# Kernel tuning notes

Measured on AMD Instinct MI355X. Metric: run time of the kernel, lower is better.

## Reference

```python
import jax, jax.numpy as jnp
import numpy as np

B, N, C, DK, TOPK = 4, 4096, 256, 64, 8


def setup_inputs() -> dict:
    key = jax.random.key(0)
    k1, k2, k3 = jax.random.split(key, 3)
    x = jax.random.normal(k1, (B, N, C), dtype=jnp.float32)
    # nn.Linear(channels, d_k, bias=False) weights, stored as [C, DK] for x @ W
    W_q = jax.random.normal(k2, (C, DK), dtype=jnp.float32) * (C ** -0.5)
    W_k = jax.random.normal(k3, (C, DK), dtype=jnp.float32) * (C ** -0.5)
    return {"x": x, "W_q": W_q, "W_k": W_k, "top_k": TOPK}


def reference(x, W_q, W_k, top_k):
    d_k = W_q.shape[-1]
    scale = d_k ** -0.5
    Q = x @ W_q                                   # [B, N, DK]
    K = x @ W_k                                   # [B, N, DK]
    S = jnp.einsum('bnd,bmd->bnm', Q, K) * scale  # [B, N, N]
    _, topk_idx = jax.lax.top_k(S, top_k)         # [B, N, top_k]
    n = S.shape[-1]
    # scatter True at top-k column indices per row (mirrors torch scatter_)
    row_mask = lambda idx: jnp.zeros((n,), dtype=bool).at[idx].set(True)
    mask = jax.vmap(jax.vmap(row_mask))(topk_idx)  # [B, N, N] bool
    S_masked = jnp.where(mask, S, -jnp.inf)
    A = jax.nn.softmax(S_masked, axis=-1)
    return A
```

## Files before the change

### kernel.cpp

```cpp
#include <hip/hip_runtime.h>
#include <math.h>

#define NROW 16384
#define NCOL 4096
#define CDIM 256
#define DKDIM 64
#define SCALE 0.125f

typedef float v4f __attribute__((ext_vector_type(4)));
typedef __attribute__((ext_vector_type(8))) short short8v;
typedef __attribute__((ext_vector_type(4))) float f32x4;

__device__ __forceinline__ unsigned mono(float v) {
  unsigned u = __float_as_uint(v);
  unsigned s = (unsigned)(((int)u) >> 31);
  return u ^ (s | 0x80000000u);
}
__device__ __forceinline__ float unmono(unsigned k) {
  unsigned u = (k & 0x80000000u) ? (k ^ 0x80000000u) : ~k;
  return __uint_as_float(u);
}
__device__ __forceinline__ unsigned short f2bf(float f) {
  unsigned u = __float_as_uint(f);
  u += 0x7FFFu + ((u >> 16) & 1u);
  return (unsigned short)(u >> 16);
}
__device__ __forceinline__ unsigned umaxu(unsigned a, unsigned b) { return a > b ? a : b; }

__device__ __forceinline__ void ins8(unsigned tk[8], unsigned& tmin, int& tmpos, unsigned v) {
  #pragma unroll
  for (int j = 0; j < 8; ++j) if (j == tmpos) tk[j] = v;
  tmin = tk[0]; tmpos = 0;
  #pragma unroll
  for (int j = 1; j < 8; ++j) if (tk[j] < tmin) { tmin = tk[j]; tmpos = j; }
}
__device__ __forceinline__ unsigned umax8(const unsigned kv[8]) {
  unsigned a = umaxu(umaxu(kv[0], kv[1]), umaxu(kv[2], kv[3]));
  unsigned b = umaxu(umaxu(kv[4], kv[5]), umaxu(kv[6], kv[7]));
  return umaxu(a, b);
}
__device__ __forceinline__ void seed8r(const unsigned kv[8],
                                       unsigned tk[8], unsigned& tmin, int& tmpos) {
  #pragma unroll
  for (int j = 0; j < 8; ++j) tk[j] = kv[j];
  tmin = tk[0]; tmpos = 0;
  #pragma unroll
  for (int j = 1; j < 8; ++j) if (tk[j] < tmin) { tmin = tk[j]; tmpos = j; }
}
__device__ __forceinline__ void scan8r(const unsigned kvin[8],
                                       unsigned tk[8], unsigned& tmin, int& tmpos) {
  unsigned kv[8];
  #pragma unroll
  for (int j = 0; j < 8; ++j) kv[j] = kvin[j];
  unsigned gm = umax8(kv);
  #pragma unroll
  for (int pass = 0; pass < 2; ++pass) {
    if (__any(gm > tmin)) {
      if (gm > tmin) {
        ins8(tk, tmin, tmpos, gm);
        #pragma unroll
        for (int j = 0; j < 8; ++j) if (kv[j] == gm) kv[j] = 0u;
      }
      gm = umax8(kv);
    }
  }
  if (__any(gm > tmin)) {
    #pragma unroll
    for (int j = 0; j < 8; ++j) if (kv[j] > tmin) ins8(tk, tmin, tmpos, kv[j]);
  }
}

__device__ __forceinline__ int kswz(int row, int off) {
  return row * 512 + (off ^ (((off >> 6) & 7) << 2));
}
__device__ __forceinline__ void ld8swz(const unsigned* k, int row, int off,
                                       unsigned kv[8]) {
  uint4 ka = *(const uint4*)&k[kswz(row, off)];
  uint4 kb = *(const uint4*)&k[kswz(row, off + 4)];
  kv[0] = ka.x; kv[1] = ka.y; kv[2] = ka.z; kv[3] = ka.w;
  kv[4] = kb.x; kv[5] = kb.y; kv[6] = kb.z; kv[7] = kb.w;
}

__global__ __launch_bounds__(512, 2) void qk_proj(
    const float* __restrict__ x, const float* __restrict__ Wq,
    const float* __restrict__ Wk, float* __restrict__ Qt,
    float* __restrict__ Kt, unsigned short* __restrict__ Qh,
    unsigned short* __restrict__ Kh) {
  __shared__ float4 xs4[64][65];
  const int t = threadIdx.x;
  const int rb = blockIdx.x;
  {
    const float4* xg = (const float4*)(x + (size_t)rb * 64 * CDIM);
    #pragma unroll
    for (int i = 0; i < 8; ++i) {
      int idx = i * 512 + t;
      xs4[idx >> 6][idx & 63] = xg[idx];
    }
  }
  __syncthreads();

  const int lane = t & 63;
  const int wu = __builtin_amdgcn_readfirstlane(t >> 6);
  const int proj = wu >> 2;
  const int chunk = wu & 3;
  const float* __restrict__ Wp = proj ? Wk : Wq;

  float acc[16];
  #pragma unroll
  for (int j = 0; j < 16; ++j) acc[j] = 0.f;

  #pragma unroll 4
  for (int cs = 0; cs < 64; ++cs) {
    float4 xv = xs4[lane][cs];
    const float xc[4] = {xv.x, xv.y, xv.z, xv.w};
    #pragma unroll
    for (int i = 0; i < 4; ++i) {
      const float4* __restrict__ w4 =
          (const float4*)(Wp + (size_t)(cs * 4 + i) * DKDIM + chunk * 16);
      float4 wa = w4[0], wb = w4[1], wc = w4[2], wd = w4[3];
      float xi = xc[i];
      acc[0]  = fmaf(xi, wa.x, acc[0]);  acc[1]  = fmaf(xi, wa.y, acc[1]);
      acc[2]  = fmaf(xi, wa.z, acc[2]);  acc[3]  = fmaf(xi, wa.w, acc[3]);
      acc[4]  = fmaf(xi, wb.x, acc[4]);  acc[5]  = fmaf(xi, wb.y, acc[5]);
      acc[6]  = fmaf(xi, wb.z, acc[6]);  acc[7]  = fmaf(xi, wb.w, acc[7]);
      acc[8]  = fmaf(xi, wc.x, acc[8]);  acc[9]  = fmaf(xi, wc.y, acc[9]);
      acc[10] = fmaf(xi, wc.z, acc[10]); acc[11] = fmaf(xi, wc.w, acc[11]);
      acc[12] = fmaf(xi, wd.x, acc[12]); acc[13] = fmaf(xi, wd.y, acc[13]);
      acc[14] = fmaf(xi, wd.z, acc[14]); acc[15] = fmaf(xi, wd.w, acc[15]);
    }
  }

  const int gr = rb * 64 + lane;
  float* Of = (proj ? Kt : Qt) + (size_t)gr * 64 + chunk * 16;
  #pragma unroll
  for (int i = 0; i < 4; ++i) {
    float4 o = {acc[4 * i], acc[4 * i + 1], acc[4 * i + 2], acc[4 * i + 3]};
    ((float4*)Of)[i] = o;
  }
  unsigned short* Oh = (proj ? Kh : Qh) + (size_t)gr * 64 + chunk * 16;
  unsigned hp[8];
  #pragma unroll
  for (int i = 0; i < 8; ++i)
    hp[i] = (unsigned)f2bf(acc[2 * i]) | ((unsigned)f2bf(acc[2 * i + 1]) << 16);
  uint4 h0 = {hp[0], hp[1], hp[2], hp[3]};
  uint4 h1 = {hp[4], hp[5], hp[6], hp[7]};
  ((uint4*)Oh)[0] = h0;
  ((uint4*)Oh)[1] = h1;
}

__global__ __launch_bounds__(256, 4) void s_fused(
    const unsigned short* __restrict__ Qh, const unsigned short* __restrict__ Kh,
    const float* __restrict__ Qt, const float* __restrict__ Kt,
    float* __restrict__ out) {
  __shared__ unsigned keys[16 * 512];
  __shared__ unsigned cand[16][64];
  float (*pval)[8] = (float(*)[8])keys;
  int   (*pcol)[8] = (int(*)[8])(keys + 128);

  const int t = threadIdx.x;
  const int lane = t & 63;
  const int wu = __builtin_amdgcn_readfirstlane(t >> 6);
  const int bid = blockIdx.x;
  const int orig = (bid & 7) * 128 + (bid >> 3);
  const int blockrow = orig * 16;
  const int b = blockrow >> 12;

  const int l15 = lane & 15, lk = lane >> 4;
  const int rowg = blockrow + l15;
  const short8v a0 = *(const short8v*)(Qh + (size_t)rowg * 64 + lk * 8);
  const short8v a1 = *(const short8v*)(Qh + (size_t)rowg * 64 + lk * 8 + 32);
  const unsigned short* Kb = Kh + ((size_t)(b << 12)) * 64;

  unsigned tk[4][8]; unsigned tmin[4]; int tmpos[4];
  #pragma unroll 1
  for (int g = 0; g < 8; ++g) {
    unsigned kv[4][8];
    #pragma unroll
    for (int t8 = 0; t8 < 8; ++t8) {
      const int col = wu * 1024 + (g * 8 + t8) * 16 + l15;
      const unsigned short* kp = Kb + (size_t)col * 64 + lk * 8;
      const short8v b0 = *(const short8v*)(kp);
      const short8v b1 = *(const short8v*)(kp + 32);
      f32x4 acc = {0.f, 0.f, 0.f, 0.f};
      acc = __builtin_amdgcn_mfma_f32_16x16x32_bf16(a0, b0, acc, 0, 0, 0);
      acc = __builtin_amdgcn_mfma_f32_16x16x32_bf16(a1, b1, acc, 0, 0, 0);
      #pragma unroll
      for (int i = 0; i < 4; ++i)
        kv[i][t8] = (mono(acc[i]) & 0xFFFFF000u) | (unsigned)col;
    }
    if (g == 0) {
      #pragma unroll
      for (int i = 0; i < 4; ++i) seed8r(kv[i], tk[i], tmin[i], tmpos[i]);
    } else {
      #pragma unroll
      for (int i = 0; i < 4; ++i) scan8r(kv[i], tk[i], tmin[i], tmpos[i]);
    }
  }
  #pragma unroll
  for (int i = 0; i < 4; ++i) {
    const int row = lk * 4 + i;
    const int off = wu * 128 + l15 * 8;
    uint4 s0 = {tk[i][0], tk[i][1], tk[i][2], tk[i][3]};
    uint4 s1 = {tk[i][4], tk[i][5], tk[i][6], tk[i][7]};
    *(uint4*)&keys[kswz(row, off)] = s0;
    *(uint4*)&keys[kswz(row, off + 4)] = s1;
  }
  __syncthreads();

  if ((t & 15) < 8) {
    const int row = t >> 4, s = t & 7;
    const int base = s * 64;
    unsigned kv[8]; unsigned mt[8]; unsigned mmin; int mmpos;
    ld8swz(keys, row, base, kv);
    seed8r(kv, mt, mmin, mmpos);
    #pragma unroll
    for (int m = 1; m < 8; ++m) {
      ld8swz(keys, row, base + m * 8, kv);
      scan8r(kv, mt, mmin, mmpos);
    }
    uint4 o0 = {mt[0], mt[1], mt[2], mt[3]};
    uint4 o1 = {mt[4], mt[5], mt[6], mt[7]};
    uint4* cp = (uint4*)(&cand[row][s * 8]);
    cp[0] = o0; cp[1] = o1;
  }
  __syncthreads();

  #pragma unroll 1
  for (int p = 0; p < 4; ++p) {
    const int rr = p * 4 + wu;
    const unsigned key = cand[rr][lane];
    const int col = (int)(key & 0xFFFu);
    const float4* Kp = (const float4*)(Kt + ((size_t)((b << 12) + col)) * 64);
    const float4* Qp = (const float4*)(Qt + (size_t)(blockrow + rr) * 64);
    float s = 0.f;
    #pragma unroll
    for (int g2 = 0; g2 < 16; ++g2) {
      float4 qf = Qp[g2];
      float4 kf = Kp[g2];
      s = fmaf(qf.x, kf.x, s);
      s = fmaf(qf.y, kf.y, s);
      s = fmaf(qf.z, kf.z, s);
      s = fmaf(qf.w, kf.w, s);
    }
    unsigned kx = mono(s);
    float vals[8]; int cols[8];
    #pragma unroll
    for (int it = 0; it < 8; ++it) {
      unsigned m = kx;
      #pragma unroll
      for (int d = 1; d < 64; d <<= 1) m = umaxu(m, (unsigned)__shfl_xor((int)m, d, 64));
      unsigned long long win = __ballot(kx == m);
      int wl = (int)__ffsll(win) - 1;
      cols[it] = __shfl(col, wl, 64);
      vals[it] = unmono(m);
      if (lane == wl) kx = 0u;
    }
    float vq[8]; float sum = 0.f;
    #pragma unroll
    for (int it = 0; it < 8; ++it) { vq[it] = __expf((vals[it] - vals[0]) * SCALE); sum += vq[it]; }
    float inv = 1.f / sum;
    if (lane < 8) {
      pval[rr][lane] = vq[lane] * inv;
      pcol[rr][lane] = cols[lane];
    }
  }
  __syncthreads();

  {
    const v4f z = {0.f, 0.f, 0.f, 0.f};
    #pragma unroll 1
    for (int j = 0; j < 4; ++j) {
      const int sr = wu * 4 + j;
      v4f* orow4 = (v4f*)(out + ((size_t)(blockrow + sr) << 12));
      #pragma unroll
      for (int i = 0; i < 16; ++i)
        __builtin_nontemporal_store(z, &orow4[(size_t)i * 64 + lane]);
    }
  }
  asm volatile("s_waitcnt vmcnt(0)" ::: "memory");
  if (lane < 32) {
    const int sr = wu * 4 + (lane >> 3);
    const int q = lane & 7;
    out[((size_t)(blockrow + sr) << 12) + (size_t)pcol[sr][q]] = pval[sr][q];
  }
}

extern "C" void kernel_launch(void* const* d_in, const int* in_sizes, int n_in,
                              void* d_out, int out_size, void* d_ws, size_t ws_size,
                              hipStream_t stream) {
  const float* x  = (const float*)d_in[0];
  const float* Wq = (const float*)d_in[1];
  const float* Wk = (const float*)d_in[2];
  float* out = (float*)d_out;

  char* ws = (char*)d_ws;
  float* Qt = (float*)ws;
  float* Kt = (float*)(ws + ((size_t)4 << 20));
  unsigned short* Qh = (unsigned short*)(ws + ((size_t)8 << 20));
  unsigned short* Kh = (unsigned short*)(ws + ((size_t)10 << 20));

  qk_proj<<<dim3(NROW / 64), 512, 0, stream>>>(x, Wq, Wk, Qt, Kt, Qh, Kh);
  s_fused<<<1024, 256, 0, stream>>>(Qh, Kh, Qt, Kt, out);
}
```

Baseline: 459.7 us.

## Replace per-column top-8 scan with group-max bucketing and bucket-level candidate rescoring

Instead of keeping a running top-8 of every bf16 score per lane, each lane now records only the max of each 8-column group (128-column strided bucket) and the candidate selection works on these group maxima. The final stage picks the top 16 groups per row, then rescored 128 fp32 columns (two per lane) to extract the exact top-8. This is meant to remove the costly per-element insertion compares in the main MFMA loop. The last barrier is dropped by making each wave zero and scatter only the rows it produced itself. A true top-8 element could be missed only if more than 16 groups beat its group; the bucket-to-column mapping must match the loop's column layout.

Result: no change. 468.6 us (+1.9%).

```diff
diff --git a/kernel.cpp b/kernel.cpp
--- a/kernel.cpp
+++ b/kernel.cpp
@@ -171,13 +171,13 @@
   const short8v a1 = *(const short8v*)(Qh + (size_t)rowg * 64 + lk * 8 + 32);
   const unsigned short* Kb = Kh + ((size_t)(b << 12)) * 64;
 
-  unsigned tk[4][8]; unsigned tmin[4]; int tmpos[4];
+  unsigned okey[4][8];
   #pragma unroll 1
   for (int g = 0; g < 8; ++g) {
-    unsigned kv[4][8];
+    float om[4];
     #pragma unroll
     for (int t8 = 0; t8 < 8; ++t8) {
-      const int col = wu * 1024 + (g * 8 + t8) * 16 + l15;
+      const int col = wu * 1024 + g * 128 + t8 * 16 + l15;
       const unsigned short* kp = Kb + (size_t)col * 64 + lk * 8;
       const short8v b0 = *(const short8v*)(kp);
       const short8v b1 = *(const short8v*)(kp + 32);
@@ -186,22 +186,19 @@
       acc = __builtin_amdgcn_mfma_f32_16x16x32_bf16(a1, b1, acc, 0, 0, 0);
       #pragma unroll
       for (int i = 0; i < 4; ++i)
-        kv[i][t8] = (mono(acc[i]) & 0xFFFFF000u) | (unsigned)col;
-    }
-    if (g == 0) {
-      #pragma unroll
-      for (int i = 0; i < 4; ++i) seed8r(kv[i], tk[i], tmin[i], tmpos[i]);
-    } else {
-      #pragma unroll
-      for (int i = 0; i < 4; ++i) scan8r(kv[i], tk[i], tmin[i], tmpos[i]);
-    }
+        om[i] = (t8 == 0) ? acc[i] : fmaxf(om[i], acc[i]);
+    }
+    const unsigned oid = (unsigned)(((wu * 8 + g) << 4) | l15);
+    #pragma unroll
+    for (int i = 0; i < 4; ++i)
+      okey[i][g] = (mono(om[i]) & 0xFFFFFE00u) | oid;
   }
   #pragma unroll
   for (int i = 0; i < 4; ++i) {
     const int row = lk * 4 + i;
     const int off = wu * 128 + l15 * 8;
-    uint4 s0 = {tk[i][0], tk[i][1], tk[i][2], tk[i][3]};
-    uint4 s1 = {tk[i][4], tk[i][5], tk[i][6], tk[i][7]};
+    uint4 s0 = {okey[i][0], okey[i][1], okey[i][2], okey[i][3]};
+    uint4 s1 = {okey[i][4], okey[i][5], okey[i][6], okey[i][7]};
     *(uint4*)&keys[kswz(row, off)] = s0;
     *(uint4*)&keys[kswz(row, off + 4)] = s1;
   }
@@ -228,32 +225,48 @@
   #pragma unroll 1
   for (int p = 0; p < 4; ++p) {
     const int rr = p * 4 + wu;
-    const unsigned key = cand[rr][lane];
-    const int col = (int)(key & 0xFFFu);
-    const float4* Kp = (const float4*)(Kt + ((size_t)((b << 12) + col)) * 64);
+    unsigned ok = cand[rr][lane];
+    const int q2 = lane >> 2, e2 = lane & 3;
+    unsigned mykey = 0u;
+    #pragma unroll
+    for (int it = 0; it < 16; ++it) {
+      unsigned m = ok;
+      #pragma unroll
+      for (int d = 1; d < 64; d <<= 1) m = umaxu(m, (unsigned)__shfl_xor((int)m, d, 64));
+      if (q2 == it) mykey = m;
+      if (ok == m) ok = 0u;
+    }
+    const unsigned oid = mykey & 0x1FFu;
+    const int colb = (int)((oid >> 4) * 128 + (oid & 15u));
+    const int col0 = colb + e2 * 16;
+    const int col1 = col0 + 64;
+    const float4* Kp0 = (const float4*)(Kt + ((size_t)((b << 12) + col0)) * 64);
+    const float4* Kp1 = (const float4*)(Kt + ((size_t)((b << 12) + col1)) * 64);
     const float4* Qp = (const float4*)(Qt + (size_t)(blockrow + rr) * 64);
-    float s = 0.f;
+    float s0 = 0.f, s1 = 0.f;
     #pragma unroll
     for (int g2 = 0; g2 < 16; ++g2) {
       float4 qf = Qp[g2];
-      float4 kf = Kp[g2];
-      s = fmaf(qf.x, kf.x, s);
-      s = fmaf(qf.y, kf.y, s);
-      s = fmaf(qf.z, kf.z, s);
-      s = fmaf(qf.w, kf.w, s);
-    }
-    unsigned kx = mono(s);
+      float4 k0f = Kp0[g2];
+      float4 k1f = Kp1[g2];
+      s0 = fmaf(qf.x, k0f.x, s0); s1 = fmaf(qf.x, k1f.x, s1);
+      s0 = fmaf(qf.y, k0f.y, s0); s1 = fmaf(qf.y, k1f.y, s1);
+      s0 = fmaf(qf.z, k0f.z, s0); s1 = fmaf(qf.z, k1f.z, s1);
+      s0 = fmaf(qf.w, k0f.w, s0); s1 = fmaf(qf.w, k1f.w, s1);
+    }
+    unsigned k0 = mono(s0), k1 = mono(s1);
     float vals[8]; int cols[8];
     #pragma unroll
     for (int it = 0; it < 8; ++it) {
-      unsigned m = kx;
+      unsigned m = umaxu(k0, k1);
       #pragma unroll
       for (int d = 1; d < 64; d <<= 1) m = umaxu(m, (unsigned)__shfl_xor((int)m, d, 64));
-      unsigned long long win = __ballot(kx == m);
+      unsigned long long win = __ballot(k0 == m || k1 == m);
       int wl = (int)__ffsll(win) - 1;
-      cols[it] = __shfl(col, wl, 64);
+      int mycol = (k0 == m) ? col0 : col1;
+      cols[it] = __shfl(mycol, wl, 64);
       vals[it] = unmono(m);
-      if (lane == wl) kx = 0u;
+      if (lane == wl) { if (k0 == m) k0 = 0u; else k1 = 0u; }
     }
     float vq[8]; float sum = 0.f;
     #pragma unroll
@@ -264,13 +277,12 @@
       pcol[rr][lane] = cols[lane];
     }
   }
-  __syncthreads();
 
   {
     const v4f z = {0.f, 0.f, 0.f, 0.f};
     #pragma unroll 1
     for (int j = 0; j < 4; ++j) {
-      const int sr = wu * 4 + j;
+      const int sr = wu + 4 * j;
       v4f* orow4 = (v4f*)(out + ((size_t)(blockrow + sr) << 12));
       #pragma unroll
       for (int i = 0; i < 16; ++i)
@@ -279,7 +291,7 @@
   }
   asm volatile("s_waitcnt vmcnt(0)" ::: "memory");
   if (lane < 32) {
-    const int sr = wu * 4 + (lane >> 3);
+    const int sr = wu + 4 * (lane >> 3);
     const int q = lane & 7;
     out[((size_t)(blockrow + sr) << 12) + (size_t)pcol[sr][q]] = pval[sr][q];
   }
```
